# Optimization experiments

Measured on AMD Instinct MI355X. Metric: run time of the kernel, lower is better.

Reference implementation:

```python
import jax, jax.numpy as jnp
import numpy as np

B, S, VOCAB, E, H, T = 256, 512, 50000, 256, 256, 32
PAD = VOCAB - 1  # mask = sentences != vocab_size - 1 in the original


def setup_inputs() -> dict:
    key = jax.random.key(0)
    ks = jax.random.split(key, 16)
    lengths = jnp.sort(jax.random.randint(ks[0], (B,), S // 2, S + 1))[::-1]
    lengths = lengths.at[0].set(S)  # sorted descending, max length present
    sentences = jax.random.randint(ks[1], (B, S), 0, VOCAB - 1)
    pos = jnp.arange(S)
    sentences = jnp.where(pos[None, :] < lengths[:, None], sentences, PAD)
    tags = jax.random.randint(ks[2], (B, S), 0, T)
    sc = jnp.float32(0.1)
    p = lambda k, shp: jax.random.normal(k, shp, jnp.float32) * sc
    return {
        'embed_table': p(ks[3], (VOCAB + 1, E)),
        'W_ih_f': p(ks[4], (4 * H, E)), 'W_hh_f': p(ks[5], (4 * H, H)),
        'b_ih_f': p(ks[6], (4 * H,)), 'b_hh_f': p(ks[7], (4 * H,)),
        'W_ih_b': p(ks[8], (4 * H, E)), 'W_hh_b': p(ks[9], (4 * H, H)),
        'b_ih_b': p(ks[10], (4 * H,)), 'b_hh_b': p(ks[11], (4 * H,)),
        'W_out': p(ks[12], (T, 2 * H)), 'b_out': p(ks[13], (T,)),
        'transition': jax.random.normal(ks[14], (T, T), jnp.float32),
        'sentences': sentences, 'tags': tags, 'sen_lengths': lengths,
    }


def _run_lstm(x_sbe, W_ih, W_hh, b_ih, b_hh):
    # x_sbe: [S, B, E]; torch gate order i, f, g, o
    Bsz, Hd = x_sbe.shape[1], W_hh.shape[1]
    gx = jnp.einsum('sbe,ge->sbg', x_sbe, W_ih) + b_ih + b_hh  # precompute input gates
    def step(carry, g):
        h, c = carry
        g = g + h @ W_hh.T
        i, f, gg, o = jnp.split(g, 4, axis=-1)
        c = jax.nn.sigmoid(f) * c + jax.nn.sigmoid(i) * jnp.tanh(gg)
        h = jax.nn.sigmoid(o) * jnp.tanh(c)
        return (h, c), h
    h0 = jnp.zeros((Bsz, Hd), x_sbe.dtype)
    _, hs = jax.lax.scan(step, (h0, h0), gx)
    return hs  # [S, B, H]


def _forward(embed_table, W_ih_f, W_hh_f, b_ih_f, b_hh_f,
             W_ih_b, W_hh_b, b_ih_b, b_hh_b, W_out, b_out, transition,
             sentences, tags, sen_lengths):
    mask = sentences != PAD                      # [B, S]
    x = embed_table[sentences]                   # [B, S, E]
    pos = jnp.arange(S)
    valid = pos[None, :] < sen_lengths[:, None]  # [B, S]
    # per-sequence reversal index (packed-sequence-faithful backward direction)
    idx = jnp.where(valid, sen_lengths[:, None] - 1 - pos[None, :], pos[None, :])
    h_f = _run_lstm(x.transpose(1, 0, 2), W_ih_f, W_hh_f, b_ih_f, b_hh_f).transpose(1, 0, 2)
    x_rev = jnp.take_along_axis(x, idx[:, :, None], axis=1)
    h_b = _run_lstm(x_rev.transpose(1, 0, 2), W_ih_b, W_hh_b, b_ih_b, b_hh_b).transpose(1, 0, 2)
    h_b = jnp.take_along_axis(h_b, idx[:, :, None], axis=1)
    h = jnp.concatenate([h_f, h_b], -1) * valid[:, :, None]  # pad_packed pads with zeros
    emit = h @ W_out.T + b_out                   # [B, S, T]; dropout is identity (eval)
    # ---- CRF negative log-likelihood ----
    fmask = mask.astype(emit.dtype)
    real = jnp.take_along_axis(emit, tags[:, :, None], axis=2)[..., 0]  # [B, S]
    real = real.at[:, 1:].add(transition[tags[:, :-1], tags[:, 1:]])
    real_score = (real * fmask).sum(axis=1)      # [B]
    def crf_step(alpha, inp):
        e_i, m_i = inp                           # [B, T], [B]
        scores = alpha[:, :, None] + transition[None, :, :] + e_i[:, None, :]
        new = jax.nn.logsumexp(scores, axis=1)
        return jnp.where(m_i[:, None], new, alpha), None
    alpha0 = emit[:, 0]                          # [B, T]
    xs = (emit[:, 1:].transpose(1, 0, 2), mask[:, 1:].T)
    alpha, _ = jax.lax.scan(crf_step, alpha0, xs)
    log_z = jax.nn.logsumexp(alpha, axis=1)      # [B]
    return -(real_score - log_z)                 # per-example loss [B]


def reference(embed_table, W_ih_f, W_hh_f, b_ih_f, b_hh_f,
              W_ih_b, W_hh_b, b_ih_b, b_hh_b, W_out, b_out, transition,
              sentences, tags, sen_lengths):
    return _forward(embed_table, W_ih_f, W_hh_f, b_ih_f, b_hh_f,
                    W_ih_b, W_hh_b, b_ih_b, b_hh_b, W_out, b_out, transition,
                    sentences, tags, sen_lengths)
```

## Files before the change

### kernel.cpp

```cpp
#include <hip/hip_runtime.h>
#include <hip/hip_bf16.h>


typedef __bf16 bf16x8 __attribute__((ext_vector_type(8)));
typedef float f32x4 __attribute__((ext_vector_type(4)));
typedef unsigned int uint4v __attribute__((ext_vector_type(4)));

__device__ __forceinline__ unsigned short f2bf(float f) {
  union { float f; unsigned int u; } v; v.f = f;
  unsigned int r = v.u + 0x7fffu + ((v.u >> 16) & 1u);
  return (unsigned short)(r >> 16);
}
__device__ __forceinline__ float bf2f(unsigned int lo16) {
  union { unsigned int u; float f; } v; v.u = lo16 << 16;
  return v.f;
}
__device__ __forceinline__ float fsig(float x) {
  float e = __builtin_amdgcn_exp2f(-1.4426950408889634f * x);
  return __builtin_amdgcn_rcpf(1.0f + e);
}
__device__ __forceinline__ float ftanh(float x) {
  float e = __builtin_amdgcn_exp2f(2.8853900817779268f * x);
  return 1.0f - 2.0f * __builtin_amdgcn_rcpf(e + 1.0f);
}

__device__ __forceinline__ void wait_ge(int* p, int target) {
  if (threadIdx.x == 0) {
    while (__hip_atomic_load(p, __ATOMIC_RELAXED, __HIP_MEMORY_SCOPE_AGENT) < target)
      __builtin_amdgcn_s_sleep(2);
    (void)__hip_atomic_load(p, __ATOMIC_ACQUIRE, __HIP_MEMORY_SCOPE_AGENT);
  }
  __syncthreads();
}

__device__ __forceinline__ void lds_barrier() {
  asm volatile("s_waitcnt lgkmcnt(0)\n\ts_barrier" ::: "memory");
}

__global__ void cvt_weights(const float* __restrict__ wih_f, const float* __restrict__ wih_b,
                            const float* __restrict__ whh_f, const float* __restrict__ whh_b,
                            const float* __restrict__ wo,
                            unsigned short* __restrict__ wih,
                            unsigned char* __restrict__ whh8,
                            unsigned char* __restrict__ wout8,
                            int* __restrict__ flags) {
  if (blockIdx.x == 0) {
    for (int f = threadIdx.x; f < 544; f += 256) flags[f] = 0;
  }
  int t = blockIdx.x * 256 + threadIdx.x;
  int i = t * 4;
  if (i < 524288) {
    const float* src = (i < 262144) ? wih_f : wih_b;
    f32x4 v = *(const f32x4*)(src + (i & 262143));
    uint2 p;
    p.x = f2bf(v[0]) | ((unsigned int)f2bf(v[1]) << 16);
    p.y = f2bf(v[2]) | ((unsigned int)f2bf(v[3]) << 16);
    *(uint2*)(wih + i) = p;
  } else if (i < 1048576) {
    int k = i - 524288;
    const float* src = (k < 262144) ? whh_f : whh_b;
    f32x4 v = *(const f32x4*)(src + (k & 262143));
    int r = 0;
    r = __builtin_amdgcn_cvt_pk_fp8_f32(v[0], v[1], r, false);
    r = __builtin_amdgcn_cvt_pk_fp8_f32(v[2], v[3], r, true);
    *(unsigned int*)(whh8 + k) = (unsigned int)r;
  } else if (i < 1064960) {
    int k = i - 1048576;
    f32x4 v = *(const f32x4*)(wo + k);
    int r = 0;
    r = __builtin_amdgcn_cvt_pk_fp8_f32(v[0], v[1], r, false);
    r = __builtin_amdgcn_cvt_pk_fp8_f32(v[2], v[3], r, true);
    *(unsigned int*)(wout8 + k) = (unsigned int)r;
  }
}


__device__ void gemm_role(
    const float* __restrict__ emb, const int* __restrict__ sent, const int* __restrict__ lens,
    const unsigned short* __restrict__ wih,
    const float* __restrict__ bih_f, const float* __restrict__ bhh_f,
    const float* __restrict__ bih_b, const float* __restrict__ bhh_b,
    unsigned short* __restrict__ gx, int* flags,
    unsigned short* wtile, float* btile)
{
  int gb = blockIdx.x - 32;
  int tid = threadIdx.x, w = tid >> 6, lane = tid & 63, col = lane & 15, q = lane >> 4;
  int ns = w >> 2, cg = w & 3;
  int prev_chunk = -1;

  for (int idx = gb; idx < 4096; idx += 224) {
    int k = idx >> 8, t = idx & 255;
    int ss = t >> 6, rest = t & 63;
    int dir = (rest >> 5) & 1, nc = (rest >> 2) & 7, bt = rest & 3;
    if (k != prev_chunk) {
      prev_chunk = k;
      if (k >= 2) wait_ge(&flags[512 + k - 2], 32);
    }
    int n0 = nc * 128, bbase = bt * 64;
    int sbase = k * 32 + ss * 8;

    if (sbase < lens[bbase]) {
      const unsigned short* wsrc = wih + (size_t)dir * 262144;
#pragma unroll
      for (int it = 0; it < 8; it++) {
        int seg = it * 512 + tid;
        int row = seg >> 5, kc = (seg & 31) * 8;
        *(uint4v*)(wtile + row * 264 + kc) = *(const uint4v*)(wsrc + (size_t)(n0 + row) * 256 + kc);
      }
      const float* bi = dir ? bih_b : bih_f;
      const float* bh = dir ? bhh_b : bhh_f;
      if (tid < 128) btile[tid] = bi[n0 + tid] + bh[n0 + tid];
      __syncthreads();

      bf16x8 wf[8][4];
#pragma unroll
      for (int kt = 0; kt < 8; kt++)
#pragma unroll
        for (int nt = 0; nt < 4; nt++)
          wf[kt][nt] = *(const bf16x8*)(wtile + (ns * 64 + nt * 16 + col) * 264 + kt * 32 + q * 8);
      f32x4 bias[4];
#pragma unroll
      for (int nt = 0; nt < 4; nt++)
#pragma unroll
        for (int rr = 0; rr < 4; rr++)
          bias[nt][rr] = btile[ns * 64 + nt * 16 + q * 4 + rr];

      int bidx = bbase + cg * 16 + col;
      int len = lens[bidx];
      const int* srow = sent + bidx * 512;

      for (int i = 0; i < 8; i++) {
        int s = sbase + i;
        int s_eff = dir ? ((s < len) ? (len - 1 - s) : s) : s;
        int token = srow[s_eff];
        const float* ep = emb + (size_t)token * 256;
        bf16x8 xf[8];
#pragma unroll
        for (int kt = 0; kt < 8; kt++) {
          f32x4 a0 = *(const f32x4*)(ep + kt * 32 + q * 8);
          f32x4 a1 = *(const f32x4*)(ep + kt * 32 + q * 8 + 4);
          uint4v pk;
          pk[0] = f2bf(a0[0]) | ((unsigned int)f2bf(a0[1]) << 16);
          pk[1] = f2bf(a0[2]) | ((unsigned int)f2bf(a0[3]) << 16);
          pk[2] = f2bf(a1[0]) | ((unsigned int)f2bf(a1[1]) << 16);
          pk[3] = f2bf(a1[2]) | ((unsigned int)f2bf(a1[3]) << 16);
          xf[kt] = __builtin_bit_cast(bf16x8, pk);
        }
        f32x4 acc[4];
#pragma unroll
        for (int nt = 0; nt < 4; nt++) acc[nt] = bias[nt];
#pragma unroll
        for (int kt = 0; kt < 8; kt++)
#pragma unroll
          for (int nt = 0; nt < 4; nt++)
            acc[nt] = __builtin_amdgcn_mfma_f32_16x16x32_bf16(wf[kt][nt], xf[kt], acc[nt], 0, 0, 0);
        size_t off = (size_t)(k & 1) * 16777216 + (size_t)dir * 8388608
                   + (size_t)(s - k * 32) * 262144 + (size_t)bidx * 1024 + n0 + ns * 64;
#pragma unroll
        for (int nt = 0; nt < 4; nt++) {
          uint2 pk;
          pk.x = f2bf(acc[nt][0]) | ((unsigned int)f2bf(acc[nt][1]) << 16);
          pk.y = f2bf(acc[nt][2]) | ((unsigned int)f2bf(acc[nt][3]) << 16);
          *(uint2*)(gx + off + nt * 16 + q * 4) = pk;
        }
      }
    }
    __syncthreads();
    if (tid == 0)
      __hip_atomic_fetch_add(&flags[k * 32 + ss * 8 + dir * 4 + bt], 1,
                             __ATOMIC_RELEASE, __HIP_MEMORY_SCOPE_AGENT);
  }
}

__device__ void lstm_role(
    const unsigned short* __restrict__ gx,
    const unsigned char* __restrict__ whh8,
    const unsigned char* __restrict__ wout8,
    const float* __restrict__ bout,
    const int* __restrict__ lens,
    unsigned short* __restrict__ emit_f, unsigned short* __restrict__ emit_b,
    int* flags, unsigned char (*hb4)[16 * 264])
{
  int bx = blockIdx.x;
  int dir = bx & 1, grp = bx >> 1, b0 = grp * 16;
  int bt = grp >> 2;
  int tid = threadIdx.x, w = tid >> 6, lane = tid & 63, col = lane & 15, q = lane >> 4;
  int maxlen = lens[b0];
  int bcl = b0 + col;
  int mylen = lens[bcl];

  const unsigned char* whb = whh8 + (size_t)dir * 262144;
  long wh[8][8];
#pragma unroll
  for (int kt = 0; kt < 8; kt++)
#pragma unroll
    for (int t = 0; t < 8; t++) {
      int row0 = (t & 3) * 256 + w * 32 + (t >> 2) * 16;
      wh[kt][t] = *(const long*)(whb + (size_t)(row0 + col) * 256 + kt * 32 + q * 8);
    }

  long wo8[8];
  f32x4 bo4 = (f32x4){0.f, 0.f, 0.f, 0.f};
#pragma unroll
  for (int kt = 0; kt < 8; kt++)
    wo8[kt] = *(const long*)(wout8 + (size_t)((w & 1) * 16 + col) * 512 + dir * 256 + kt * 32 + q * 8);
  if (dir == 0) {
#pragma unroll
    for (int r = 0; r < 4; r++) bo4[r] = bout[(w & 1) * 16 + q * 4 + r];
  }
  unsigned short* ebase = dir ? emit_b : emit_f;

  float c8[8];
  long hf8[8];
#pragma unroll
  for (int i = 0; i < 8; i++) { c8[i] = 0.f; hf8[i] = 0; }

  for (int c = 0; c < 16; c++) {
    int s0 = c * 32;
    if (s0 < maxlen) {
      int cend = s0 + 32; if (cend > maxlen) cend = maxlen;
      const unsigned short* gbase = gx + (size_t)(c & 1) * 16777216 + (size_t)dir * 8388608
                                       + (size_t)bcl * 1024 + q * 4;
      for (int ss = 0; ss < 4; ss++) {
        int sp0 = s0 + ss * 8;
        if (sp0 >= maxlen) break;
        int spe = sp0 + 8; if (spe > cend) spe = cend;
        wait_ge(&flags[c * 32 + ss * 8 + dir * 4 + bt], 8);

        uint2 gxr[8];
        {
          const unsigned short* gf = gbase + (size_t)(sp0 - s0) * 262144;
#pragma unroll
          for (int t = 0; t < 8; t++) {
            int row0 = (t & 3) * 256 + w * 32 + (t >> 2) * 16;
            gxr[t] = *(const uint2*)(gf + row0);
          }
        }

        for (int s = sp0; s < spe; s++) {
          f32x4 acc[8];
#pragma unroll
          for (int t = 0; t < 8; t++) {
            f32x4 a;
            a[0] = bf2f(gxr[t].x & 0xffffu); a[1] = bf2f(gxr[t].x >> 16);
            a[2] = bf2f(gxr[t].y & 0xffffu); a[3] = bf2f(gxr[t].y >> 16);
            acc[t] = a;
          }
          if (s + 1 < spe) {
            const unsigned short* gn = gbase + (size_t)(s + 1 - s0) * 262144;
#pragma unroll
            for (int t = 0; t < 8; t++) {
              int row0 = (t & 3) * 256 + w * 32 + (t >> 2) * 16;
              gxr[t] = *(const uint2*)(gn + row0);
            }
          }
#pragma unroll
          for (int kt = 0; kt < 8; kt++) {
            long hv8 = hf8[kt];
#pragma unroll
            for (int t = 0; t < 8; t++)
              acc[t] = __builtin_amdgcn_mfma_f32_16x16x32_fp8_fp8(wh[kt][t], hv8, acc[t], 0, 0, 0);
          }
          float hv[8];
#pragma unroll
          for (int a = 0; a < 2; a++)
#pragma unroll
            for (int r = 0; r < 4; r++) {
              float ig = acc[a * 4 + 0][r], fg = acc[a * 4 + 1][r];
              float gg = acc[a * 4 + 2][r], og = acc[a * 4 + 3][r];
              float cn = fsig(fg) * c8[a * 4 + r] + fsig(ig) * ftanh(gg);
              c8[a * 4 + r] = cn;
              hv[a * 4 + r] = fsig(og) * ftanh(cn);
            }
          int par = s & 7;
#pragma unroll
          for (int a = 0; a < 2; a++) {
            int r8 = 0;
            r8 = __builtin_amdgcn_cvt_pk_fp8_f32(hv[a * 4 + 0], hv[a * 4 + 1], r8, false);
            r8 = __builtin_amdgcn_cvt_pk_fp8_f32(hv[a * 4 + 2], hv[a * 4 + 3], r8, true);
            *(unsigned int*)(&hb4[par][col * 264 + w * 32 + a * 16 + q * 4]) = (unsigned int)r8;
          }
          lds_barrier();
#pragma unroll
          for (int kt = 0; kt < 8; kt++)
            hf8[kt] = *(const long*)(&hb4[par][col * 264 + kt * 32 + q * 8]);

          if ((s & 3) == 3 || s == spe - 1) {
            int ebeg = s & ~3;
            int e = ebeg + (w >> 1);
            if (e <= s) {
              f32x4 ea = bo4;
#pragma unroll
              for (int kt = 0; kt < 8; kt++) {
                long hbv = *(const long*)(&hb4[e & 7][col * 264 + kt * 32 + q * 8]);
                ea = __builtin_amdgcn_mfma_f32_16x16x32_fp8_fp8(wo8[kt], hbv, ea, 0, 0, 0);
              }
              if (e < mylen) {
                int pos = dir ? (mylen - 1 - e) : e;
                uint2 pk;
                pk.x = f2bf(ea[0]) | ((unsigned int)f2bf(ea[1]) << 16);
                pk.y = f2bf(ea[2]) | ((unsigned int)f2bf(ea[3]) << 16);
                *(uint2*)(ebase + (((size_t)bcl * 512 + pos) * 32 + (w & 1) * 16 + q * 4)) = pk;
              }
            }
          }
        }
      }
    }
    __syncthreads();
    if (tid == 0)
      __hip_atomic_fetch_add(&flags[512 + c], 1, __ATOMIC_RELEASE, __HIP_MEMORY_SCOPE_AGENT);
  }
}

__global__ __launch_bounds__(512, 2) void fused_persist(
    const float* __restrict__ emb, const int* __restrict__ sent, const int* __restrict__ lens,
    const unsigned short* __restrict__ wih,
    const float* __restrict__ bih_f, const float* __restrict__ bhh_f,
    const float* __restrict__ bih_b, const float* __restrict__ bhh_b,
    unsigned short* __restrict__ gx,
    const unsigned char* __restrict__ whh8, const unsigned char* __restrict__ wout8,
    const float* __restrict__ bout,
    unsigned short* __restrict__ emit_f, unsigned short* __restrict__ emit_b,
    int* flags)
{
  __shared__ __align__(16) unsigned short wtile[128 * 264];
  __shared__ __align__(16) float btile[128];
  __shared__ __align__(16) unsigned char hb4[8][16 * 264];

  if (blockIdx.x < 32) {
    lstm_role(gx, whh8, wout8, bout, lens, emit_f, emit_b, flags, hb4);
  } else {
    gemm_role(emb, sent, lens, wih, bih_f, bhh_f, bih_b, bhh_b, gx, flags, wtile, btile);
  }
}

__global__ __launch_bounds__(64) void crf_kernel(
    const unsigned short* __restrict__ emit_f,
    const unsigned short* __restrict__ emit_b,
    const float* __restrict__ trans, const int* __restrict__ tags,
    const int* __restrict__ lens, float* __restrict__ out) {
  const float LOG2E = 1.4426950408889634f, LN2 = 0.6931471805599453f;
  __shared__ __align__(16) float e_lds[512 * 32];
  int b = blockIdx.x, lane = threadIdx.x;
  int len = lens[b];
  const int* tg = tags + b * 512;

  size_t ebase = (size_t)b * 512 * 32;
  const unsigned short* pf = emit_f + ebase;
  const unsigned short* pb = emit_b + ebase;
  int ng = len * 4;
  for (int g = lane; g < ng; g += 64) {
    uint4v fv = *(const uint4v*)(pf + g * 8);
    uint4v bv = *(const uint4v*)(pb + g * 8);
    f32x4 w0, w1;
#pragma unroll
    for (int k = 0; k < 2; k++) {
      w0[2 * k]     = (bf2f(fv[k] & 0xffffu) + bf2f(bv[k] & 0xffffu)) * LOG2E;
      w0[2 * k + 1] = (bf2f(fv[k] >> 16)     + bf2f(bv[k] >> 16))     * LOG2E;
      w1[2 * k]     = (bf2f(fv[k + 2] & 0xffffu) + bf2f(bv[k + 2] & 0xffffu)) * LOG2E;
      w1[2 * k + 1] = (bf2f(fv[k + 2] >> 16)     + bf2f(bv[k + 2] >> 16))     * LOG2E;
    }
    *(f32x4*)(e_lds + g * 8) = w0;
    *(f32x4*)(e_lds + g * 8 + 4) = w1;
  }
  __syncthreads();

  float rs2 = 0.f, rst = 0.f;
  for (int s = lane; s < len; s += 64) {
    int t1 = tg[s];
    rs2 += e_lds[s * 32 + t1];
    if (s > 0) rst += trans[tg[s - 1] * 32 + t1];
  }
  float rsc = LN2 * rs2 + rst;
#pragma unroll
  for (int m = 32; m; m >>= 1) rsc += __shfl_xor(rsc, m);

  int j = lane & 31, half = lane >> 5, i0 = half * 16;
  float tr2[16];
  int pidx[16];
#pragma unroll
  for (int ii = 0; ii < 16; ii++) {
    tr2[ii] = trans[(i0 + ii) * 32 + j] * LOG2E;
    pidx[ii] = (i0 + ii) << 2;
  }
  const float* ep = e_lds + j;
  float B = ep[0];
  float e_nxt = ep[32];
  for (int s = 1; s < len; s++) {
    float e_cur = e_nxt;
    int sn = (s + 1 < len) ? (s + 1) : s;
    e_nxt = ep[sn * 32];
    float v[16];
#pragma unroll
    for (int ii = 0; ii < 16; ii++)
      v[ii] = __builtin_bit_cast(float, __builtin_amdgcn_ds_bpermute(
                  pidx[ii], __builtin_bit_cast(int, B))) + tr2[ii];
    float a8[8], a4[4], a2[2];
#pragma unroll
    for (int ii = 0; ii < 8; ii++) a8[ii] = fmaxf(v[ii], v[ii + 8]);
#pragma unroll
    for (int ii = 0; ii < 4; ii++) a4[ii] = fmaxf(a8[ii], a8[ii + 4]);
    a2[0] = fmaxf(a4[0], a4[2]); a2[1] = fmaxf(a4[1], a4[3]);
    float m1 = fmaxf(a2[0], a2[1]);
    float m2 = fmaxf(m1, __shfl_xor(m1, 32));
    float x[16];
#pragma unroll
    for (int ii = 0; ii < 16; ii++) x[ii] = __builtin_amdgcn_exp2f(v[ii] - m2);
    float s8[8], s4[4], s2[2];
#pragma unroll
    for (int ii = 0; ii < 8; ii++) s8[ii] = x[ii] + x[ii + 8];
#pragma unroll
    for (int ii = 0; ii < 4; ii++) s4[ii] = s8[ii] + s8[ii + 4];
    s2[0] = s4[0] + s4[2]; s2[1] = s4[1] + s4[3];
    float sum = s2[0] + s2[1];
    sum += __shfl_xor(sum, 32);
    B = m2 + __builtin_amdgcn_logf(sum) + e_cur;
  }
  float mz = B;
#pragma unroll
  for (int m = 16; m; m >>= 1) mz = fmaxf(mz, __shfl_xor(mz, m));
  float sz = __builtin_amdgcn_exp2f(B - mz);
#pragma unroll
  for (int m = 16; m; m >>= 1) sz += __shfl_xor(sz, m);
  float logz = LN2 * (mz + __builtin_amdgcn_logf(sz));
  if (lane == 0) out[b] = logz - rsc;
}

extern "C" void kernel_launch(void* const* d_in, const int* in_sizes, int n_in,
                              void* d_out, int out_size, void* d_ws, size_t ws_size,
                              hipStream_t stream) {
  const float* emb   = (const float*)d_in[0];
  const float* Wih_f = (const float*)d_in[1];
  const float* Whh_f = (const float*)d_in[2];
  const float* bih_f = (const float*)d_in[3];
  const float* bhh_f = (const float*)d_in[4];
  const float* Wih_b = (const float*)d_in[5];
  const float* Whh_b = (const float*)d_in[6];
  const float* bih_b = (const float*)d_in[7];
  const float* bhh_b = (const float*)d_in[8];
  const float* Wout  = (const float*)d_in[9];
  const float* bout  = (const float*)d_in[10];
  const float* trans = (const float*)d_in[11];
  const int* sent = (const int*)d_in[12];
  const int* tags = (const int*)d_in[13];
  const int* lens = (const int*)d_in[14];
  float* out = (float*)d_out;

  char* ws = (char*)d_ws;
  if (ws_size < 87048192ull) return;
  unsigned short* gx      = (unsigned short*)(ws);
  unsigned short* emit_f  = (unsigned short*)(ws + 67108864);
  unsigned short* emit_b  = (unsigned short*)(ws + 75497472);
  unsigned short* wih_bf  = (unsigned short*)(ws + 83886080);
  unsigned char*  whh8    = (unsigned char*)(ws + 84934656);
  unsigned char*  wout8   = (unsigned char*)(ws + 85458944);
  int*            flags   = (int*)(ws + 85475328);

  cvt_weights<<<1040, 256, 0, stream>>>(Wih_f, Wih_b, Whh_f, Whh_b, Wout,
                                        wih_bf, whh8, wout8, flags);
  fused_persist<<<256, 512, 0, stream>>>(
      emb, sent, lens, wih_bf, bih_f, bhh_f, bih_b, bhh_b, gx,
      whh8, wout8, bout, emit_f, emit_b, flags);
  crf_kernel<<<256, 64, 0, stream>>>(emit_f, emit_b, trans, tags, lens, out);
}
```

Before: 1.545 ms.

## Fuse LSTM gate reciprocals, swizzle h LDS layout, pack two sequences per CRF wave

The LSTM cell math now merges each sigmoid-times-tanh product into a single reciprocal, clamping the exponent argument to avoid overflow. This cuts transcendental and rcp instructions on the serial recurrence path. The fp8 hidden-state LDS buffer is XOR-swizzled by column to reduce bank conflicts on the per-step reads and writes. The CRF kernel now runs two sequences per 64-lane wave, each half handling all 32 source tags, which removes the cross-half shuffles but doubles the per-lane bpermute and exp work and halves the grid.

Result: slower. 1.725 ms (+11.6%).

```diff
diff --git a/kernel.cpp b/kernel.cpp
--- a/kernel.cpp
+++ b/kernel.cpp
@@ -14,14 +14,6 @@
 __device__ __forceinline__ float bf2f(unsigned int lo16) {
   union { unsigned int u; float f; } v; v.u = lo16 << 16;
   return v.f;
-}
-__device__ __forceinline__ float fsig(float x) {
-  float e = __builtin_amdgcn_exp2f(-1.4426950408889634f * x);
-  return __builtin_amdgcn_rcpf(1.0f + e);
-}
-__device__ __forceinline__ float ftanh(float x) {
-  float e = __builtin_amdgcn_exp2f(2.8853900817779268f * x);
-  return 1.0f - 2.0f * __builtin_amdgcn_rcpf(e + 1.0f);
 }
 
 __device__ __forceinline__ void wait_ge(int* p, int target) {
@@ -188,6 +180,7 @@
   int maxlen = lens[b0];
   int bcl = b0 + col;
   int mylen = lens[bcl];
+  int c7 = col & 7;
 
   const unsigned char* whb = whh8 + (size_t)dir * 262144;
   long wh[8][8];
@@ -214,6 +207,9 @@
   long hf8[8];
 #pragma unroll
   for (int i = 0; i < 8; i++) { c8[i] = 0.f; hf8[i] = 0; }
+
+  const float NK  = -1.4426950408889634f;
+  const float N2K = -2.8853900817779268f;
 
   for (int c = 0; c < 16; c++) {
     int s0 = c * 32;
@@ -268,9 +264,15 @@
             for (int r = 0; r < 4; r++) {
               float ig = acc[a * 4 + 0][r], fg = acc[a * 4 + 1][r];
               float gg = acc[a * 4 + 2][r], og = acc[a * 4 + 3][r];
-              float cn = fsig(fg) * c8[a * 4 + r] + fsig(ig) * ftanh(gg);
+              float ui = __builtin_amdgcn_exp2f(NK * ig);
+              float uf = __builtin_amdgcn_exp2f(NK * fg);
+              float uo = __builtin_amdgcn_exp2f(NK * og);
+              float tg = __builtin_amdgcn_exp2f(fminf(N2K * gg, 80.0f));
+              float cf = c8[a * 4 + r] * __builtin_amdgcn_rcpf(1.0f + uf);
+              float cn = cf + (1.0f - tg) * __builtin_amdgcn_rcpf((1.0f + ui) * (1.0f + tg));
               c8[a * 4 + r] = cn;
-              hv[a * 4 + r] = fsig(og) * ftanh(cn);
+              float tc = __builtin_amdgcn_exp2f(fminf(N2K * cn, 80.0f));
+              hv[a * 4 + r] = (1.0f - tc) * __builtin_amdgcn_rcpf((1.0f + uo) * (1.0f + tc));
             }
           int par = s & 7;
 #pragma unroll
@@ -278,12 +280,12 @@
             int r8 = 0;
             r8 = __builtin_amdgcn_cvt_pk_fp8_f32(hv[a * 4 + 0], hv[a * 4 + 1], r8, false);
             r8 = __builtin_amdgcn_cvt_pk_fp8_f32(hv[a * 4 + 2], hv[a * 4 + 3], r8, true);
-            *(unsigned int*)(&hb4[par][col * 264 + w * 32 + a * 16 + q * 4]) = (unsigned int)r8;
+            *(unsigned int*)(&hb4[par][col * 264 + ((w ^ c7) * 32 + a * 16 + q * 4)]) = (unsigned int)r8;
           }
           lds_barrier();
 #pragma unroll
           for (int kt = 0; kt < 8; kt++)
-            hf8[kt] = *(const long*)(&hb4[par][col * 264 + kt * 32 + q * 8]);
+            hf8[kt] = *(const long*)(&hb4[par][col * 264 + ((kt ^ c7) * 32 + q * 8)]);
 
           if ((s & 3) == 3 || s == spe - 1) {
             int ebeg = s & ~3;
@@ -292,7 +294,7 @@
               f32x4 ea = bo4;
 #pragma unroll
               for (int kt = 0; kt < 8; kt++) {
-                long hbv = *(const long*)(&hb4[e & 7][col * 264 + kt * 32 + q * 8]);
+                long hbv = *(const long*)(&hb4[e & 7][col * 264 + ((kt ^ c7) * 32 + q * 8)]);
                 ea = __builtin_amdgcn_mfma_f32_16x16x32_fp8_fp8(wo8[kt], hbv, ea, 0, 0, 0);
               }
               if (e < mylen) {
@@ -341,81 +343,84 @@
     const float* __restrict__ trans, const int* __restrict__ tags,
     const int* __restrict__ lens, float* __restrict__ out) {
   const float LOG2E = 1.4426950408889634f, LN2 = 0.6931471805599453f;
-  __shared__ __align__(16) float e_lds[512 * 32];
-  int b = blockIdx.x, lane = threadIdx.x;
-  int len = lens[b];
-  const int* tg = tags + b * 512;
-
-  size_t ebase = (size_t)b * 512 * 32;
-  const unsigned short* pf = emit_f + ebase;
-  const unsigned short* pb = emit_b + ebase;
-  int ng = len * 4;
-  for (int g = lane; g < ng; g += 64) {
-    uint4v fv = *(const uint4v*)(pf + g * 8);
-    uint4v bv = *(const uint4v*)(pb + g * 8);
-    f32x4 w0, w1;
-#pragma unroll
-    for (int k = 0; k < 2; k++) {
-      w0[2 * k]     = (bf2f(fv[k] & 0xffffu) + bf2f(bv[k] & 0xffffu)) * LOG2E;
-      w0[2 * k + 1] = (bf2f(fv[k] >> 16)     + bf2f(bv[k] >> 16))     * LOG2E;
-      w1[2 * k]     = (bf2f(fv[k + 2] & 0xffffu) + bf2f(bv[k + 2] & 0xffffu)) * LOG2E;
-      w1[2 * k + 1] = (bf2f(fv[k + 2] >> 16)     + bf2f(bv[k + 2] >> 16))     * LOG2E;
+  __shared__ __align__(16) float e_lds[2][16384];
+  int lane = threadIdx.x, half = lane >> 5, j = lane & 31;
+  int b0 = blockIdx.x * 2, sb = b0 + half;
+  int mylen = lens[sb];
+
+#pragma unroll
+  for (int ssn = 0; ssn < 2; ssn++) {
+    int b = b0 + ssn;
+    int ng = lens[b] * 4;
+    const unsigned short* pf = emit_f + (size_t)b * 16384;
+    const unsigned short* pb = emit_b + (size_t)b * 16384;
+    float* dst = e_lds[ssn];
+    for (int g = lane; g < ng; g += 64) {
+      uint4v fv = *(const uint4v*)(pf + g * 8);
+      uint4v bv = *(const uint4v*)(pb + g * 8);
+      f32x4 w0, w1;
+#pragma unroll
+      for (int k = 0; k < 2; k++) {
+        w0[2 * k]     = (bf2f(fv[k] & 0xffffu) + bf2f(bv[k] & 0xffffu)) * LOG2E;
+        w0[2 * k + 1] = (bf2f(fv[k] >> 16)     + bf2f(bv[k] >> 16))     * LOG2E;
+        w1[2 * k]     = (bf2f(fv[k + 2] & 0xffffu) + bf2f(bv[k + 2] & 0xffffu)) * LOG2E;
+        w1[2 * k + 1] = (bf2f(fv[k + 2] >> 16)     + bf2f(bv[k + 2] >> 16))     * LOG2E;
+      }
+      *(f32x4*)(dst + g * 8) = w0;
+      *(f32x4*)(dst + g * 8 + 4) = w1;
     }
-    *(f32x4*)(e_lds + g * 8) = w0;
-    *(f32x4*)(e_lds + g * 8 + 4) = w1;
   }
   __syncthreads();
 
+  const int* tg_ = tags + sb * 512;
   float rs2 = 0.f, rst = 0.f;
-  for (int s = lane; s < len; s += 64) {
-    int t1 = tg[s];
-    rs2 += e_lds[s * 32 + t1];
-    if (s > 0) rst += trans[tg[s - 1] * 32 + t1];
+  for (int s = j; s < mylen; s += 32) {
+    int t1 = tg_[s];
+    rs2 += e_lds[half][s * 32 + t1];
+    if (s > 0) rst += trans[tg_[s - 1] * 32 + t1];
   }
   float rsc = LN2 * rs2 + rst;
 #pragma unroll
-  for (int m = 32; m; m >>= 1) rsc += __shfl_xor(rsc, m);
-
-  int j = lane & 31, half = lane >> 5, i0 = half * 16;
-  float tr2[16];
-  int pidx[16];
-#pragma unroll
-  for (int ii = 0; ii < 16; ii++) {
-    tr2[ii] = trans[(i0 + ii) * 32 + j] * LOG2E;
-    pidx[ii] = (i0 + ii) << 2;
-  }
-  const float* ep = e_lds + j;
+  for (int m = 16; m; m >>= 1) rsc += __shfl_xor(rsc, m);
+
+  float tr2[32];
+#pragma unroll
+  for (int ii = 0; ii < 32; ii++) tr2[ii] = trans[ii * 32 + j] * LOG2E;
+  int pb32 = (lane & 32) << 2;
+  const float* ep = e_lds[half] + j;
   float B = ep[0];
   float e_nxt = ep[32];
-  for (int s = 1; s < len; s++) {
+  for (int s = 1; s < mylen; s++) {
     float e_cur = e_nxt;
-    int sn = (s + 1 < len) ? (s + 1) : s;
+    int sn = (s + 1 < mylen) ? (s + 1) : s;
     e_nxt = ep[sn * 32];
-    float v[16];
-#pragma unroll
-    for (int ii = 0; ii < 16; ii++)
+    float v[32];
+#pragma unroll
+    for (int ii = 0; ii < 32; ii++)
       v[ii] = __builtin_bit_cast(float, __builtin_amdgcn_ds_bpermute(
-                  pidx[ii], __builtin_bit_cast(int, B))) + tr2[ii];
-    float a8[8], a4[4], a2[2];
-#pragma unroll
-    for (int ii = 0; ii < 8; ii++) a8[ii] = fmaxf(v[ii], v[ii + 8]);
+                  pb32 + ii * 4, __builtin_bit_cast(int, B))) + tr2[ii];
+    float a16[16], a8[8], a4[4], a2[2];
+#pragma unroll
+    for (int ii = 0; ii < 16; ii++) a16[ii] = fmaxf(v[ii], v[ii + 16]);
+#pragma unroll
+    for (int ii = 0; ii < 8; ii++) a8[ii] = fmaxf(a16[ii], a16[ii + 8]);
 #pragma unroll
     for (int ii = 0; ii < 4; ii++) a4[ii] = fmaxf(a8[ii], a8[ii + 4]);
     a2[0] = fmaxf(a4[0], a4[2]); a2[1] = fmaxf(a4[1], a4[3]);
     float m1 = fmaxf(a2[0], a2[1]);
-    float m2 = fmaxf(m1, __shfl_xor(m1, 32));
-    float x[16];
-#pragma unroll
-    for (int ii = 0; ii < 16; ii++) x[ii] = __builtin_amdgcn_exp2f(v[ii] - m2);
-    float s8[8], s4[4], s2[2];
-#pragma unroll
-    for (int ii = 0; ii < 8; ii++) s8[ii] = x[ii] + x[ii + 8];
+    float x[32];
+#pragma unroll
+    for (int ii = 0; ii < 32; ii++) x[ii] = __builtin_amdgcn_exp2f(v[ii] - m1);
+    float s16[16], s8[8], s4[4], s2[2];
+#pragma unroll
+    for (int ii = 0; ii < 16; ii++) s16[ii] = x[ii] + x[ii + 16];
+#pragma unroll
+    for (int ii = 0; ii < 8; ii++) s8[ii] = s16[ii] + s16[ii + 8];
 #pragma unroll
     for (int ii = 0; ii < 4; ii++) s4[ii] = s8[ii] + s8[ii + 4];
     s2[0] = s4[0] + s4[2]; s2[1] = s4[1] + s4[3];
     float sum = s2[0] + s2[1];
-    sum += __shfl_xor(sum, 32);
-    B = m2 + __builtin_amdgcn_logf(sum) + e_cur;
+    B = m1 + __builtin_amdgcn_logf(sum) + e_cur;
   }
   float mz = B;
 #pragma unroll
@@ -424,7 +429,7 @@
 #pragma unroll
   for (int m = 16; m; m >>= 1) sz += __shfl_xor(sz, m);
   float logz = LN2 * (mz + __builtin_amdgcn_logf(sz));
-  if (lane == 0) out[b] = logz - rsc;
+  if (j == 0) out[sb] = logz - rsc;
 }
 
 extern "C" void kernel_launch(void* const* d_in, const int* in_sizes, int n_in,
@@ -462,5 +467,5 @@
   fused_persist<<<256, 512, 0, stream>>>(
       emb, sent, lens, wih_bf, bih_f, bhh_f, bih_b, bhh_b, gx,
       whh8, wout8, bout, emit_f, emit_b, flags);
-  crf_kernel<<<256, 64, 0, stream>>>(emit_f, emit_b, trans, tags, lens, out);
-}
+  crf_kernel<<<128, 64, 0, stream>>>(emit_f, emit_b, trans, tags, lens, out);
+}
```
